# Performance work log

Measured on AMD Instinct MI355X. Metric: run time of the kernel, lower is better.

Reference implementation:

```python
import jax, jax.numpy as jnp
import numpy as np
import math

B, S, D, H, HD, DC, FF, E, K = 4, 2048, 576, 9, 64, 64, 1536, 8, 2
EPS = 1e-6


def _rms(x):
    # RMSNorm with weight=ones (module instantiates a fresh RMSNorm in forward)
    return x / jnp.sqrt(jnp.mean(x * x, axis=-1, keepdims=True) + EPS)


def _expert(h, wa, wb, wc):
    return (jax.nn.gelu(h @ wa, approximate=False) * (h @ wc)) @ wb


def _forward(x, q_w, kv_w, o_w, gate_w, w1, w2, w3, sw1, sw2, sw3):
    # ---------------- MLA ----------------
    xn = _rms(x)
    q = (xn @ q_w).reshape(B, S, H, HD)
    kv = (xn @ kv_w).reshape(B, S, H, 2 * DC)
    k, v = kv[..., :DC], kv[..., DC:]
    # RoPE (complex-pair form) applied to q only, as in the source
    theta = 1.0 / (10000.0 ** (jnp.arange(0, HD, 2, dtype=jnp.float32) / HD))
    freqs = jnp.arange(S, dtype=jnp.float32)[:, None] * theta[None, :]  # [S, HD/2]
    cos = jnp.cos(freqs)[None, :, None, :]
    sin = jnp.sin(freqs)[None, :, None, :]
    qp = q.reshape(B, S, H, HD // 2, 2)
    qe, qo = qp[..., 0], qp[..., 1]
    q = jnp.stack([qe * cos - qo * sin, qe * sin + qo * cos], axis=-1).reshape(B, S, H, HD)
    # NOTE: source matmul attends head-vs-head per token: [B,S,H,HD] x [B,S,DC,H] -> [B,S,H,H]
    attn = jnp.einsum('bshd,bstd->bsht', q, k) / math.sqrt(HD)
    attn = jax.nn.softmax(attn, axis=-1)
    ao = jnp.einsum('bsht,bstd->bshd', attn, v)  # [B,S,H,DC]
    # faithful to torch: transpose(1,2).contiguous().view(B,S,D)
    ao = ao.transpose(0, 2, 1, 3).reshape(B, S, D)
    x = ao @ o_w + x
    # ---------------- MoE ----------------
    xn = _rms(x)
    gw = jax.nn.softmax(xn @ gate_w, axis=-1)  # [B,S,E]
    tw, ti = jax.lax.top_k(gw, K)
    tw = tw / jnp.sum(tw, axis=-1, keepdims=True)
    # combine weights per expert: zero for unselected experts (same math as masked loop)
    comb = jnp.sum(tw[..., None] * jax.nn.one_hot(ti, E, dtype=x.dtype), axis=-2)  # [B,S,E]
    h1 = jax.nn.gelu(jnp.einsum('bsd,edf->ebsf', xn, w1), approximate=False)
    h3 = jnp.einsum('bsd,edf->ebsf', xn, w3)
    eo = jnp.einsum('ebsf,efd->ebsd', h1 * h3, w2)  # [E,B,S,D]
    moe_out = jnp.einsum('ebsd,bse->bsd', eo, comb)
    shared = _expert(xn, sw1, sw2, sw3)
    return moe_out + shared + x


def setup_inputs() -> dict:
    key = jax.random.key(0)
    ks = jax.random.split(key, 11)
    s = 0.02
    return {
        'x': jax.random.normal(ks[0], (B, S, D), dtype=jnp.float32),
        'q_w': jax.random.normal(ks[1], (D, D), dtype=jnp.float32) * s,
        'kv_w': jax.random.normal(ks[2], (D, H * 2 * DC), dtype=jnp.float32) * s,
        'o_w': jax.random.normal(ks[3], (D, D), dtype=jnp.float32) * s,
        'gate_w': jax.random.normal(ks[4], (D, E), dtype=jnp.float32) * s,
        'w1': jax.random.normal(ks[5], (E, D, FF), dtype=jnp.float32) * s,
        'w2': jax.random.normal(ks[6], (E, FF, D), dtype=jnp.float32) * s,
        'w3': jax.random.normal(ks[7], (E, D, FF), dtype=jnp.float32) * s,
        'sw1': jax.random.normal(ks[8], (D, FF), dtype=jnp.float32) * s,
        'sw2': jax.random.normal(ks[9], (FF, D), dtype=jnp.float32) * s,
        'sw3': jax.random.normal(ks[10], (D, FF), dtype=jnp.float32) * s,
    }


def reference(x, q_w, kv_w, o_w, gate_w, w1, w2, w3, sw1, sw2, sw3):
    return _forward(x, q_w, kv_w, o_w, gate_w, w1, w2, w3, sw1, sw2, sw3)
```

## Files before the change

kernel.cpp:

```cpp
#include <hip/hip_runtime.h>
#include <math.h>

#define B_  4
#define S_  2048
#define D_  576
#define H_  9
#define HD_ 64
#define FF_ 1536
#define E_  8
#define TOK (B_*S_)
#define T1ROWS 17408
#define T1ALL  25600

typedef unsigned int   u32x4  __attribute__((ext_vector_type(4)));
typedef unsigned short u16x8  __attribute__((ext_vector_type(8)));
typedef __bf16         bf16x8 __attribute__((ext_vector_type(8)));
typedef _Float16       f16x8  __attribute__((ext_vector_type(8)));
typedef float          f32x4  __attribute__((ext_vector_type(4)));

__device__ __forceinline__ float b2f(unsigned short u) {
    union { unsigned int i; float f; } v; v.i = ((unsigned int)u) << 16; return v.f;
}
__device__ __forceinline__ unsigned short f2b(float f) {
    unsigned int u = __builtin_bit_cast(unsigned int, f);
    unsigned int r = 0x7fffu + ((u >> 16) & 1u);
    return (unsigned short)((u + r) >> 16);
}

__global__ __launch_bounds__(256)
void rmsnorm_k(const float* __restrict__ x, unsigned short* __restrict__ xn) {
    int tok = blockIdx.x, tid = threadIdx.x;
    const float* xr = x + (size_t)tok * D_;
    float v0 = xr[tid];
    float v1 = xr[tid + 256];
    float v2 = (tid < D_ - 512) ? xr[tid + 512] : 0.f;
    float ss = v0*v0 + v1*v1 + v2*v2;
    #pragma unroll
    for (int d = 1; d < 64; d <<= 1) ss += __shfl_xor(ss, d, 64);
    __shared__ float red[4];
    if ((tid & 63) == 0) red[tid >> 6] = ss;
    __syncthreads();
    float tot = red[0] + red[1] + red[2] + red[3];
    float rms = rsqrtf(tot / (float)D_ + 1e-6f);
    unsigned short* orow = xn + (size_t)tok * D_;
    orow[tid]       = f2b(v0 * rms);
    orow[tid + 256] = f2b(v1 * rms);
    if (tid < D_ - 512) orow[tid + 512] = f2b(v2 * rms);
}

__global__ __launch_bounds__(256)
void rms32_k(const float* __restrict__ x, float* __restrict__ xn) {
    int tok = blockIdx.x, tid = threadIdx.x;
    const float* xr = x + (size_t)tok * D_;
    float v0 = xr[tid];
    float v1 = xr[tid + 256];
    float v2 = (tid < D_ - 512) ? xr[tid + 512] : 0.f;
    float ss = v0*v0 + v1*v1 + v2*v2;
    #pragma unroll
    for (int d = 1; d < 64; d <<= 1) ss += __shfl_xor(ss, d, 64);
    __shared__ float red[4];
    if ((tid & 63) == 0) red[tid >> 6] = ss;
    __syncthreads();
    float tot = red[0] + red[1] + red[2] + red[3];
    float rms = rsqrtf(tot / (float)D_ + 1e-6f);
    float* orow = xn + (size_t)tok * D_;
    orow[tid]       = v0 * rms;
    orow[tid + 256] = v1 * rms;
    if (tid < D_ - 512) orow[tid + 512] = v2 * rms;
}

__global__ __launch_bounds__(256)
void convw13_k(const float* __restrict__ w1, const float* __restrict__ w3,
               const float* __restrict__ sw1, const float* __restrict__ sw3,
               unsigned short* __restrict__ wt1, unsigned short* __restrict__ wt3)
{
    const size_t WE = (size_t)D_ * FF_;
    int z = blockIdx.z;
    const float* s; unsigned short* d;
    if (z < 8)       { s = w1 + (size_t)z * WE;       d = wt1 + (size_t)z * WE; }
    else if (z == 8) { s = sw1;                        d = wt1 + 8 * WE; }
    else if (z < 17) { s = w3 + (size_t)(z - 9) * WE;  d = wt3 + (size_t)(z - 9) * WE; }
    else             { s = sw3;                        d = wt3 + 8 * WE; }
    const int K = D_, N = FF_;
    __shared__ unsigned short t[64][72];
    int n0 = blockIdx.x * 64, k0 = blockIdx.y * 64;
    int tx = threadIdx.x & 63, ty = threadIdx.x >> 6;
    #pragma unroll
    for (int i = 0; i < 16; ++i) {
        int k = i * 4 + ty;
        t[k][tx] = f2b(s[(size_t)(k0 + k) * N + n0 + tx]);
    }
    __syncthreads();
    int r = threadIdx.x >> 3, c8 = (threadIdx.x & 7) * 8;
    #pragma unroll
    for (int it = 0; it < 2; ++it, r += 32) {
        u16x8 v;
        #pragma unroll
        for (int j = 0; j < 8; ++j) v[j] = t[c8 + j][r];
        *(u16x8*)&d[(size_t)(n0 + r) * K + k0 + c8] = v;
    }
}

__global__ __launch_bounds__(256)
void convw2_k(const float* __restrict__ w2, const float* __restrict__ sw2,
              unsigned short* __restrict__ wt2)
{
    const size_t WE = (size_t)D_ * FF_;
    int z = blockIdx.z;
    const float* s = (z < 8) ? w2 + (size_t)z * WE : sw2;
    unsigned short* d = wt2 + (size_t)z * WE;
    const int K = FF_, N = D_;
    __shared__ unsigned short t[64][72];
    int n0 = blockIdx.x * 64, k0 = blockIdx.y * 64;
    int tx = threadIdx.x & 63, ty = threadIdx.x >> 6;
    #pragma unroll
    for (int i = 0; i < 16; ++i) {
        int k = i * 4 + ty;
        t[k][tx] = f2b(s[(size_t)(k0 + k) * N + n0 + tx]);
    }
    __syncthreads();
    int r = threadIdx.x >> 3, c8 = (threadIdx.x & 7) * 8;
    #pragma unroll
    for (int it = 0; it < 2; ++it, r += 32) {
        u16x8 v;
        #pragma unroll
        for (int j = 0; j < 8; ++j) v[j] = t[c8 + j][r];
        *(u16x8*)&d[(size_t)(n0 + r) * K + k0 + c8] = v;
    }
}

__global__ __launch_bounds__(256)
void convS_k(const float* __restrict__ src,
             _Float16* __restrict__ dh, _Float16* __restrict__ dl,
             int K, int N)
{
    __shared__ _Float16 th[64][72], tl[64][72];
    int n0 = blockIdx.x * 64, k0 = blockIdx.y * 64;
    int tx = threadIdx.x & 63, ty = threadIdx.x >> 6;
    #pragma unroll
    for (int i = 0; i < 16; ++i) {
        int k = i * 4 + ty;
        float v = src[(size_t)(k0 + k) * N + n0 + tx];
        _Float16 h = (_Float16)v;
        th[k][tx] = h;
        tl[k][tx] = (_Float16)((v - (float)h) * 2048.0f);
    }
    __syncthreads();
    int r = threadIdx.x >> 3, c8 = (threadIdx.x & 7) * 8;
    #pragma unroll
    for (int it = 0; it < 2; ++it, r += 32) {
        f16x8 vh, vl;
        #pragma unroll
        for (int j = 0; j < 8; ++j) { vh[j] = th[c8 + j][r]; vl[j] = tl[c8 + j][r]; }
        *(f16x8*)&dh[(size_t)(n0 + r) * K + k0 + c8] = vh;
        *(f16x8*)&dl[(size_t)(n0 + r) * K + k0 + c8] = vl;
    }
}

template<int BN, int EPI, int WB>
__global__ __launch_bounds__(256)
void gemmS_k(const float* __restrict__ A, const float* __restrict__ Bm,
             const _Float16* __restrict__ Bhp, const _Float16* __restrict__ Blp,
             float* __restrict__ Cout, const float* __restrict__ resid,
             int M, int N, int K, int ldb)
{
    constexpr int BM = 128, BK = 64;
    constexpr int WM = BM / 2, WN = BN / 2, MI = WM / 16, NJ = WN / 16;
    __shared__ alignas(16) _Float16 Ah[BM][BK], Al[BM][BK];
    __shared__ alignas(16) _Float16 Bh[BN][BK], Bl[BN][BK];
    const int tid  = threadIdx.x;
    const int bn0  = blockIdx.x * BN, bm0 = blockIdx.y * BM;
    const int lane = tid & 63, wave = tid >> 6;
    const int l    = lane & 15, quad = lane >> 4;
    const int wm   = wave >> 1, wn = wave & 1;
    const int rsz  = (l & 7) << 3;

    f32x4 accH[MI][NJ], accL[MI][NJ];
    #pragma unroll
    for (int mi = 0; mi < MI; ++mi)
        #pragma unroll
        for (int nj = 0; nj < NJ; ++nj) {
            accH[mi][nj] = (f32x4){0.f, 0.f, 0.f, 0.f};
            accL[mi][nj] = (f32x4){0.f, 0.f, 0.f, 0.f};
        }

    const int nK = K / BK;
    for (int kc = 0; kc < nK; ++kc) {
        __syncthreads();
        #pragma unroll
        for (int i = 0; i < (BM * BK) / 2048; ++i) {
            int u = i * 256 + tid;
            int r = u >> 3, c8 = (u & 7) * 8;
            int cs = c8 ^ ((r & 7) << 3);
            const float* ga = A + (size_t)(bm0 + r) * K + kc * BK + c8;
            f16x8 hh, ll;
            #pragma unroll
            for (int j = 0; j < 8; ++j) {
                float v = ga[j];
                _Float16 h = (_Float16)v;
                hh[j] = h;
                ll[j] = (_Float16)((v - (float)h) * 2048.0f);
            }
            *(f16x8*)&Ah[r][cs] = hh;
            *(f16x8*)&Al[r][cs] = ll;
        }
        if constexpr (WB == 1) {
            #pragma unroll
            for (int i = 0; i < (BN * BK) / 2048; ++i) {
                int u = i * 256 + tid;
                int n = u >> 3, c8 = (u & 7) * 8;
                int cs = c8 ^ ((n & 7) << 3);
                *(f16x8*)&Bh[n][cs] =
                    *(const f16x8*)(Bhp + (size_t)(bn0 + n) * K + kc * BK + c8);
                *(f16x8*)&Bl[n][cs] =
                    *(const f16x8*)(Blp + (size_t)(bn0 + n) * K + kc * BK + c8);
            }
        } else {
            #pragma unroll
            for (int i = 0; i < (BN * BK) / 2048; ++i) {
                int u = i * 256 + tid;
                int n = u % BN, k8 = (u / BN) * 8;
                int cs = k8 ^ ((n & 7) << 3);
                const float* gB = Bm + (size_t)(kc * BK + k8) * ldb + bn0 + n;
                f16x8 hh, ll;
                #pragma unroll
                for (int j = 0; j < 8; ++j) {
                    float v = gB[(size_t)j * ldb];
                    _Float16 h = (_Float16)v;
                    hh[j] = h;
                    ll[j] = (_Float16)((v - (float)h) * 2048.0f);
                }
                *(f16x8*)&Bh[n][cs] = hh;
                *(f16x8*)&Bl[n][cs] = ll;
            }
        }
        __syncthreads();
        #pragma unroll
        for (int ks = 0; ks < BK; ks += 32) {
            f16x8 ah[MI], al[MI], bh[NJ], bl[NJ];
            int col = (ks + quad * 8) ^ rsz;
            #pragma unroll
            for (int mi = 0; mi < MI; ++mi) {
                ah[mi] = *(const f16x8*)&Ah[wm * WM + mi * 16 + l][col];
                al[mi] = *(const f16x8*)&Al[wm * WM + mi * 16 + l][col];
            }
            #pragma unroll
            for (int nj = 0; nj < NJ; ++nj) {
                bh[nj] = *(const f16x8*)&Bh[wn * WN + nj * 16 + l][col];
                bl[nj] = *(const f16x8*)&Bl[wn * WN + nj * 16 + l][col];
            }
            #pragma unroll
            for (int mi = 0; mi < MI; ++mi)
                #pragma unroll
                for (int nj = 0; nj < NJ; ++nj) {
                    accH[mi][nj] = __builtin_amdgcn_mfma_f32_16x16x32_f16(
                        ah[mi], bh[nj], accH[mi][nj], 0, 0, 0);
                    accL[mi][nj] = __builtin_amdgcn_mfma_f32_16x16x32_f16(
                        ah[mi], bl[nj], accL[mi][nj], 0, 0, 0);
                    accL[mi][nj] = __builtin_amdgcn_mfma_f32_16x16x32_f16(
                        al[mi], bh[nj], accL[mi][nj], 0, 0, 0);
                }
        }
    }
    #pragma unroll
    for (int mi = 0; mi < MI; ++mi)
        #pragma unroll
        for (int nj = 0; nj < NJ; ++nj)
            #pragma unroll
            for (int r = 0; r < 4; ++r) {
                int row = bm0 + wm * WM + mi * 16 + quad * 4 + r;
                int col = bn0 + wn * WN + nj * 16 + l;
                float v = accH[mi][nj][r] + accL[mi][nj][r] * (1.0f / 2048.0f);
                size_t idx = (size_t)row * N + col;
                if constexpr (EPI == 0) Cout[idx] = v;
                else                    Cout[idx] = v + resid[idx];
            }
}

__global__ __launch_bounds__(256, 2)
void gemm13_k(const unsigned short* __restrict__ A,
              const unsigned short* __restrict__ B1,
              const unsigned short* __restrict__ B3,
              unsigned short* __restrict__ T1o,
              const int* __restrict__ eidx,
              const int* __restrict__ counts,
              const int* __restrict__ offs,
              int N, long long bstr)
{
    constexpr int BM = 128, BK = 64;
    constexpr int MI = 4, NJ = 4;
    __shared__ alignas(16) unsigned short As[BM][BK];
    __shared__ alignas(16) unsigned short Bs1[BM][BK];
    __shared__ alignas(16) unsigned short Bs3[BM][BK];
    __shared__ int rowbuf[BM];
    const int tid  = threadIdx.x;
    const int bn0  = blockIdx.x * 128, bm0 = blockIdx.y * 128;
    const int lane = tid & 63, wave = tid >> 6;
    const int l    = lane & 15, quad = lane >> 4;
    const int wm   = wave >> 1, wn = wave & 1;
    const int rs   = tid >> 3, c8 = (tid & 7) * 8;
    const int wsz  = (rs & 7) << 3;
    const int rsz  = (l & 7) << 3;

    int e = blockIdx.z;
    int cnt = counts[e];
    if (bm0 >= cnt) return;
    int crow0 = offs[e];
    B1 += (long long)e * bstr;
    B3 += (long long)e * bstr;
    if (tid < BM) {
        int rr = bm0 + tid;
        rowbuf[tid] = (rr < cnt) ? eidx[e * TOK + rr] : 0;
    }
    __syncthreads();

    f32x4 acc1[MI][NJ], acc3[MI][NJ];
    #pragma unroll
    for (int mi = 0; mi < MI; ++mi)
        #pragma unroll
        for (int nj = 0; nj < NJ; ++nj) {
            acc1[mi][nj] = (f32x4){0.f, 0.f, 0.f, 0.f};
            acc3[mi][nj] = (f32x4){0.f, 0.f, 0.f, 0.f};
        }

    const int nK = D_ / BK;
    u32x4 ra[4], rb1[4], rb3[4];
    #pragma unroll
    for (int i = 0; i < 4; ++i) {
        int r = i * 32 + rs;
        int arow = rowbuf[r];
        ra[i]  = *(const u32x4*)(A  + (size_t)arow * D_ + c8);
        rb1[i] = *(const u32x4*)(B1 + (size_t)(bn0 + r) * D_ + c8);
        rb3[i] = *(const u32x4*)(B3 + (size_t)(bn0 + r) * D_ + c8);
    }
    for (int kc = 0; kc < nK; ++kc) {
        __syncthreads();
        #pragma unroll
        for (int i = 0; i < 4; ++i) {
            int r = i * 32 + rs;
            *(u32x4*)&As[r][c8 ^ wsz]  = ra[i];
            *(u32x4*)&Bs1[r][c8 ^ wsz] = rb1[i];
            *(u32x4*)&Bs3[r][c8 ^ wsz] = rb3[i];
        }
        __syncthreads();
        if (kc + 1 < nK) {
            int ko = (kc + 1) * BK;
            #pragma unroll
            for (int i = 0; i < 4; ++i) {
                int r = i * 32 + rs;
                int arow = rowbuf[r];
                ra[i]  = *(const u32x4*)(A  + (size_t)arow * D_ + ko + c8);
                rb1[i] = *(const u32x4*)(B1 + (size_t)(bn0 + r) * D_ + ko + c8);
                rb3[i] = *(const u32x4*)(B3 + (size_t)(bn0 + r) * D_ + ko + c8);
            }
        }
        #pragma unroll
        for (int ks = 0; ks < BK; ks += 32) {
            bf16x8 af[MI], b1f[NJ], b3f[NJ];
            int col = (ks + quad * 8) ^ rsz;
            #pragma unroll
            for (int mi = 0; mi < MI; ++mi)
                af[mi] = __builtin_bit_cast(bf16x8,
                    *(const u32x4*)&As[wm * 64 + mi * 16 + l][col]);
            #pragma unroll
            for (int nj = 0; nj < NJ; ++nj) {
                b1f[nj] = __builtin_bit_cast(bf16x8,
                    *(const u32x4*)&Bs1[wn * 64 + nj * 16 + l][col]);
                b3f[nj] = __builtin_bit_cast(bf16x8,
                    *(const u32x4*)&Bs3[wn * 64 + nj * 16 + l][col]);
            }
            #pragma unroll
            for (int mi = 0; mi < MI; ++mi)
                #pragma unroll
                for (int nj = 0; nj < NJ; ++nj) {
                    acc1[mi][nj] = __builtin_amdgcn_mfma_f32_16x16x32_bf16(
                        af[mi], b1f[nj], acc1[mi][nj], 0, 0, 0);
                    acc3[mi][nj] = __builtin_amdgcn_mfma_f32_16x16x32_bf16(
                        af[mi], b3f[nj], acc3[mi][nj], 0, 0, 0);
                }
        }
    }
    #pragma unroll
    for (int mi = 0; mi < MI; ++mi)
        #pragma unroll
        for (int nj = 0; nj < NJ; ++nj)
            #pragma unroll
            for (int r = 0; r < 4; ++r) {
                int lrow = bm0 + wm * 64 + mi * 16 + quad * 4 + r;
                int col  = bn0 + wn * 64 + nj * 16 + l;
                float hv = b2f(f2b(acc1[mi][nj][r]));
                float g  = 0.5f * hv * (1.0f + erff(hv * 0.70710678118654752f));
                T1o[(size_t)(crow0 + lrow) * N + col] = f2b(g * acc3[mi][nj][r]);
            }
}

__global__ __launch_bounds__(256)
void gemm2_k(const unsigned short* __restrict__ A,
             const unsigned short* __restrict__ Bm,
             float* __restrict__ Cout,
             const float* __restrict__ wgt,
             const int* __restrict__ eidx,
             const int* __restrict__ counts,
             const int* __restrict__ offs,
             int N, int K, int ldb, long long bstr)
{
    constexpr int BM = 64, BN = 192, BK = 64;
    constexpr int MI = 2, NJ = 6;
    constexpr int AIT = (BM * BK) / 2048;
    constexpr int BIT = (BN * BK) / 2048;
    __shared__ alignas(16) unsigned short As[BM][BK];
    __shared__ alignas(16) unsigned short Bs[BN][BK];
    __shared__ int rowbuf[BM];
    const int tid  = threadIdx.x;
    const int bn0  = blockIdx.x * BN, bm0 = blockIdx.y * BM;
    const int lane = tid & 63, wave = tid >> 6;
    const int l    = lane & 15, quad = lane >> 4;
    const int wm   = wave >> 1, wn = wave & 1;
    const int rs   = tid >> 3, c8 = (tid & 7) * 8;
    const int wsz  = (rs & 7) << 3;
    const int rsz  = (l & 7) << 3;

    int e = blockIdx.z;
    int cnt = counts[e];
    if (bm0 >= cnt) return;
    int crow0 = offs[e];
    int ebase = e * TOK;
    const unsigned short* Bt = Bm + (long long)e * bstr;
    if (tid < BM) {
        int rr = bm0 + tid;
        rowbuf[tid] = (rr < cnt) ? eidx[ebase + rr] : 0;
    }

    f32x4 acc[MI][NJ];
    #pragma unroll
    for (int mi = 0; mi < MI; ++mi)
        #pragma unroll
        for (int nj = 0; nj < NJ; ++nj) acc[mi][nj] = (f32x4){0.f, 0.f, 0.f, 0.f};

    const int nK = K / BK;
    u32x4 pa[AIT], pb[BIT];
    #pragma unroll
    for (int i = 0; i < AIT; ++i) {
        int r = i * 32 + rs;
        pa[i] = *(const u32x4*)(A + (size_t)(crow0 + bm0 + r) * K + c8);
    }
    #pragma unroll
    for (int i = 0; i < BIT; ++i) {
        int n = i * 32 + rs;
        pb[i] = *(const u32x4*)(Bt + (size_t)(bn0 + n) * ldb + c8);
    }
    for (int kc = 0; kc < nK; ++kc) {
        __syncthreads();
        #pragma unroll
        for (int i = 0; i < AIT; ++i) {
            int r = i * 32 + rs;
            *(u32x4*)&As[r][c8 ^ wsz] = pa[i];
        }
        #pragma unroll
        for (int i = 0; i < BIT; ++i) {
            int n = i * 32 + rs;
            *(u32x4*)&Bs[n][c8 ^ wsz] = pb[i];
        }
        __syncthreads();
        if (kc + 1 < nK) {
            int ko = (kc + 1) * BK;
            #pragma unroll
            for (int i = 0; i < AIT; ++i) {
                int r = i * 32 + rs;
                pa[i] = *(const u32x4*)(A + (size_t)(crow0 + bm0 + r) * K + ko + c8);
            }
            #pragma unroll
            for (int i = 0; i < BIT; ++i) {
                int n = i * 32 + rs;
                pb[i] = *(const u32x4*)(Bt + (size_t)(bn0 + n) * ldb + ko + c8);
            }
        }
        #pragma unroll
        for (int ks = 0; ks < BK; ks += 32) {
            bf16x8 af[MI], bfr[NJ];
            int col = (ks + quad * 8) ^ rsz;
            #pragma unroll
            for (int mi = 0; mi < MI; ++mi)
                af[mi] = __builtin_bit_cast(bf16x8,
                    *(const u32x4*)&As[wm * 32 + mi * 16 + l][col]);
            #pragma unroll
            for (int nj = 0; nj < NJ; ++nj)
                bfr[nj] = __builtin_bit_cast(bf16x8,
                    *(const u32x4*)&Bs[wn * 96 + nj * 16 + l][col]);
            #pragma unroll
            for (int mi = 0; mi < MI; ++mi)
                #pragma unroll
                for (int nj = 0; nj < NJ; ++nj)
                    acc[mi][nj] = __builtin_amdgcn_mfma_f32_16x16x32_bf16(
                        af[mi], bfr[nj], acc[mi][nj], 0, 0, 0);
        }
    }
    #pragma unroll
    for (int mi = 0; mi < MI; ++mi)
        #pragma unroll
        for (int nj = 0; nj < NJ; ++nj)
            #pragma unroll
            for (int r = 0; r < 4; ++r) {
                int lrow = bm0 + wm * 32 + mi * 16 + quad * 4 + r;
                if (lrow < cnt) {
                    int   tok = rowbuf[lrow - bm0];
                    float sc  = wgt[ebase + lrow];
                    int   col = bn0 + wn * 96 + nj * 16 + l;
                    atomicAdd(&Cout[(size_t)tok * N + col], sc * acc[mi][nj][r]);
                }
            }
}

template<int BN, int EPI, int ROUTED, int WB>
__global__ __launch_bounds__(256)
void gemm_k(const unsigned short* __restrict__ A,
            const void* __restrict__ Bm,
            void* __restrict__ Cout,
            const void* __restrict__ resid,
            const float* __restrict__ wgt,
            const int* __restrict__ eidx,
            const int* __restrict__ counts,
            const int* __restrict__ offs,
            int M, int N, int K, int ldb, long long bstr)
{
    constexpr int BM = 128, BK = 64, LDT = BK + 8;
    constexpr int WM = BM / 2, WN = BN / 2, MI = WM / 16, NJ = WN / 16;
    constexpr int AIT = (BM * BK) / 2048, BIT = (BN * BK) / 2048;
    __shared__ alignas(16) unsigned short As[BM][LDT];
    __shared__ alignas(16) unsigned short Bs[BN][LDT];
    __shared__ int rowbuf[BM];
    const int tid  = threadIdx.x;
    const int bn0  = blockIdx.x * BN, bm0 = blockIdx.y * BM;
    const int lane = tid & 63, wave = tid >> 6;
    const int l    = lane & 15, quad = lane >> 4;
    const int wm   = wave >> 1, wn = wave & 1;

    int cnt = M, crow0 = 0, ebase = 0;
    long long boff = 0;
    if constexpr (ROUTED) {
        int e = blockIdx.z;
        cnt = counts[e];
        if (bm0 >= cnt) return;
        crow0 = offs[e];
        ebase = e * TOK;
        boff  = (long long)e * bstr;
        if (tid < BM) {
            int rr = bm0 + tid;
            rowbuf[tid] = (rr < cnt) ? eidx[ebase + rr] : 0;
        }
        __syncthreads();
    }

    f32x4 acc[MI][NJ];
    #pragma unroll
    for (int mi = 0; mi < MI; ++mi)
        #pragma unroll
        for (int nj = 0; nj < NJ; ++nj) acc[mi][nj] = (f32x4){0.f, 0.f, 0.f, 0.f};

    const int nK = K / BK;
    for (int kc = 0; kc < nK; ++kc) {
        __syncthreads();
        #pragma unroll
        for (int i = 0; i < AIT; ++i) {
            int u = i * 256 + tid;
            int r = u >> 3, c8 = (u & 7) * 8;
            int arow;
            if constexpr (ROUTED && EPI != 5) arow = rowbuf[r];
            else if constexpr (ROUTED)        arow = crow0 + bm0 + r;
            else                              arow = bm0 + r;
            *(u32x4*)&As[r][c8] =
                *(const u32x4*)(A + (size_t)arow * K + kc * BK + c8);
        }
        const float* Bf = (const float*)Bm + boff;
        #pragma unroll
        for (int i = 0; i < BIT; ++i) {
            int u = i * 256 + tid;
            int n = u % BN, k8 = (u / BN) * 8;
            const float* gB = Bf + (size_t)(kc * BK + k8) * ldb + bn0 + n;
            u16x8 tmp;
            #pragma unroll
            for (int j = 0; j < 8; ++j) tmp[j] = f2b(gB[(size_t)j * ldb]);
            *(u16x8*)&Bs[n][k8] = tmp;
        }
        __syncthreads();
        #pragma unroll
        for (int ks = 0; ks < BK; ks += 32) {
            bf16x8 af[MI], bfr[NJ];
            #pragma unroll
            for (int mi = 0; mi < MI; ++mi)
                af[mi] = __builtin_bit_cast(bf16x8,
                    *(const u32x4*)&As[wm * WM + mi * 16 + l][ks + quad * 8]);
            #pragma unroll
            for (int nj = 0; nj < NJ; ++nj)
                bfr[nj] = __builtin_bit_cast(bf16x8,
                    *(const u32x4*)&Bs[wn * WN + nj * 16 + l][ks + quad * 8]);
            #pragma unroll
            for (int mi = 0; mi < MI; ++mi)
                #pragma unroll
                for (int nj = 0; nj < NJ; ++nj)
                    acc[mi][nj] = __builtin_amdgcn_mfma_f32_16x16x32_bf16(
                        af[mi], bfr[nj], acc[mi][nj], 0, 0, 0);
        }
    }
    #pragma unroll
    for (int mi = 0; mi < MI; ++mi)
        #pragma unroll
        for (int nj = 0; nj < NJ; ++nj)
            #pragma unroll
            for (int r = 0; r < 4; ++r) {
                int lrow = bm0 + wm * WM + mi * 16 + quad * 4 + r;
                int col  = bn0 + wn * WN + nj * 16 + l;
                float v = acc[mi][nj][r];
                if constexpr (EPI == 0) {
                    ((unsigned short*)Cout)[(size_t)(crow0 + lrow) * N + col] = f2b(v);
                } else if constexpr (EPI == 3) {
                    size_t ix = (size_t)(crow0 + lrow) * N + col;
                    float hv = b2f(((const unsigned short*)resid)[ix]);
                    float g = 0.5f * hv * (1.0f + erff(hv * 0.70710678118654752f));
                    ((unsigned short*)Cout)[ix] = f2b(g * v);
                } else if constexpr (EPI == 4) {
                    ((float*)Cout)[(size_t)lrow * N + col] += v;
                } else {
                    if (lrow < cnt) {
                        int   tok = rowbuf[lrow - bm0];
                        float sc  = wgt[ebase + lrow];
                        atomicAdd(&((float*)Cout)[(size_t)tok * N + col], sc * v);
                    }
                }
            }
}

__global__ __launch_bounds__(256)
void attn32_k(const float* __restrict__ q,
              const float* __restrict__ kv,
              float* __restrict__ ao,
              int pos0)
{
    int pl   = blockIdx.x * 4 + (threadIdx.x >> 6);
    int lane = threadIdx.x & 63;
    int pos  = pos0 + pl;
    int b = pos >> 11, s = pos & 2047;

    const float* qp  = q  + (size_t)pl * 576;
    const float* kvp = kv + (size_t)pl * 1152;

    int i = lane >> 1;
    float theta = powf(10000.f, -(float)i * (1.0f / 32.0f));
    float sn, cs;
    sincosf((float)s * theta, &sn, &cs);

    float qr[H_], kr[H_], vr[H_];
    #pragma unroll
    for (int h = 0; h < H_; ++h) {
        float qv = qp[h * 64 + lane];
        float qo = __shfl_xor(qv, 1, 64);
        qr[h] = (lane & 1) ? (qo * sn + qv * cs) : (qv * cs - qo * sn);
        kr[h] = kvp[h * 128 + lane];
        vr[h] = kvp[h * 128 + 64 + lane];
    }

    #pragma unroll
    for (int h = 0; h < H_; ++h) {
        float sc[H_];
        #pragma unroll
        for (int t = 0; t < H_; ++t) {
            float p = qr[h] * kr[t];
            #pragma unroll
            for (int d = 1; d < 64; d <<= 1) p += __shfl_xor(p, d, 64);
            sc[t] = p * 0.125f;
        }
        float mx = sc[0];
        #pragma unroll
        for (int t = 1; t < H_; ++t) mx = fmaxf(mx, sc[t]);
        float ssum = 0.f;
        #pragma unroll
        for (int t = 0; t < H_; ++t) { sc[t] = __expf(sc[t] - mx); ssum += sc[t]; }
        float inv = 1.0f / ssum;
        float ov = 0.f;
        #pragma unroll
        for (int t = 0; t < H_; ++t) ov += sc[t] * vr[t];
        ao[((size_t)(b * H_ + h) * S_ + s) * 64 + lane] = ov * inv;
    }
}

__global__ __launch_bounds__(256)
void gate1_k(const float* __restrict__ x2,
             const float* __restrict__ gw,
             float* __restrict__ tw,
             int*   __restrict__ tsel)
{
    int tok  = blockIdx.x * 4 + (threadIdx.x >> 6);
    int lane = threadIdx.x & 63;
    float acc[8];
    #pragma unroll
    for (int e = 0; e < 8; ++e) acc[e] = 0.f;
    float ss = 0.f;
    for (int d = lane; d < D_; d += 64) {
        float xv = x2[(size_t)tok * D_ + d];
        ss += xv * xv;
        const float* wr = gw + (size_t)d * 8;
        #pragma unroll
        for (int e = 0; e < 8; ++e) acc[e] += xv * wr[e];
    }
    #pragma unroll
    for (int d = 1; d < 64; d <<= 1) ss += __shfl_xor(ss, d, 64);
    #pragma unroll
    for (int e = 0; e < 8; ++e)
        #pragma unroll
        for (int d = 1; d < 64; d <<= 1) acc[e] += __shfl_xor(acc[e], d, 64);
    if (lane == 0) {
        float rms = rsqrtf(ss / (float)D_ + 1e-6f);
        #pragma unroll
        for (int e = 0; e < 8; ++e) acc[e] *= rms;
        float mx = acc[0];
        #pragma unroll
        for (int e = 1; e < 8; ++e) mx = fmaxf(mx, acc[e]);
        float g[8], ssum = 0.f;
        #pragma unroll
        for (int e = 0; e < 8; ++e) { g[e] = __expf(acc[e] - mx); ssum += g[e]; }
        #pragma unroll
        for (int e = 0; e < 8; ++e) g[e] /= ssum;
        int i1 = 0;
        #pragma unroll
        for (int e = 1; e < 8; ++e) if (g[e] > g[i1]) i1 = e;
        int i2 = -1;
        #pragma unroll
        for (int e = 0; e < 8; ++e)
            if (e != i1 && (i2 < 0 || g[e] > g[i2])) i2 = e;
        float s2 = g[i1] + g[i2];
        tw[(size_t)tok * 2 + 0] = g[i1] / s2;
        tw[(size_t)tok * 2 + 1] = g[i2] / s2;
        tsel[tok] = i1 | (i2 << 8);
    }
}

__global__ __launch_bounds__(256)
void gate2_k(const int*   __restrict__ tsel,
             const float* __restrict__ tw,
             float* __restrict__ wgt,
             int*   __restrict__ eidx,
             int*   __restrict__ counts)
{
    int e    = blockIdx.x;
    int tid  = threadIdx.x;
    int lane = tid & 63, wv = tid >> 6;
    __shared__ int wtot[4];
    int base = 0;
    for (int t0 = 0; t0 < TOK; t0 += 256) {
        int tok = t0 + tid;
        int hit = 0; float w = 0.f;
        if (e == E_) { hit = 1; w = 1.0f; }
        else {
            int s = tsel[tok];
            if ((s & 255) == e)      { hit = 1; w = tw[(size_t)tok * 2 + 0]; }
            else if ((s >> 8) == e)  { hit = 1; w = tw[(size_t)tok * 2 + 1]; }
        }
        unsigned long long m = __ballot(hit);
        int pre = __popcll(m & ((1ull << lane) - 1ull));
        if (lane == 0) wtot[wv] = __popcll(m);
        __syncthreads();
        int off = base;
        for (int q = 0; q < wv; ++q) off += wtot[q];
        if (hit) {
            int p = off + pre;
            eidx[e * TOK + p] = tok;
            wgt [e * TOK + p] = w;
        }
        base += wtot[0] + wtot[1] + wtot[2] + wtot[3];
        __syncthreads();
    }
    if (tid == 0) counts[e] = base;
}

__global__ void offs_k(const int* __restrict__ counts, int* __restrict__ offs) {
    if (threadIdx.x == 0) {
        int run = 0;
        for (int e = 0; e < 9; ++e) {
            offs[e] = run;
            run += ((counts[e] + 127) >> 7) << 7;
        }
    }
}

extern "C" void kernel_launch(void* const* d_in, const int* in_sizes, int n_in,
                              void* d_out, int out_size, void* d_ws, size_t ws_size,
                              hipStream_t stream)
{
    const float* x      = (const float*)d_in[0];
    const float* q_w    = (const float*)d_in[1];
    const float* kv_w   = (const float*)d_in[2];
    const float* o_w    = (const float*)d_in[3];
    const float* gate_w = (const float*)d_in[4];
    const float* w1     = (const float*)d_in[5];
    const float* w2     = (const float*)d_in[6];
    const float* w3     = (const float*)d_in[7];
    const float* sw1    = (const float*)d_in[8];
    const float* sw2    = (const float*)d_in[9];
    const float* sw3    = (const float*)d_in[10];
    float* out = (float*)d_out;

    const size_t XN = (size_t)TOK * D_ * 2;
    char* ws = (char*)d_ws;
    unsigned short* xn16 = (unsigned short*)ws;
    float*          ao32 = (float*)(ws + XN);

    const size_t QE = (size_t)D_ * D_, KVE = (size_t)1152 * D_;
    const size_t SW = (2 * QE + KVE) * 2 * 2;
    _Float16* qwh  = (_Float16*)(ws + 3 * XN);
    _Float16* qwl  = qwh  + QE;
    _Float16* kvwh = qwl  + QE;
    _Float16* kvwl = kvwh + KVE;
    _Float16* owh  = kvwl + KVE;
    _Float16* owl  = owh  + QE;

    bool convA = true;
    int TC = -1;
    for (int pass = 0; pass < 2; ++pass) {
        size_t base = 3 * XN + (convA ? SW : 0);
        if      (base + 8*XN    <= ws_size) { TC = 1; break; }
        else if (base + 8*XN/2  <= ws_size) { TC = 2; break; }
        else if (base + 8*XN/4  <= ws_size) { TC = 4; break; }
        else if (base + 8*XN/8  <= ws_size) { TC = 8; break; }
        else if (base + 8*XN/16 <= ws_size) { TC = 16; break; }
        else if (base + 8*XN/32 <= ws_size) { TC = 32; break; }
        else if (base + 8*XN/64 <= ws_size) { TC = 64; break; }
        convA = false;
    }
    if (TC < 0) { convA = false; TC = 64; }
    const int CT = TOK / TC;
    float* xn32c = (float*)(ws + 3*XN + (convA ? SW : 0));
    float* qc    = xn32c + (size_t)CT * D_;
    float* kvc   = qc    + (size_t)CT * D_;

    int*   counts = (int*)(ws + XN);
    int*   offs   = counts + 16;
    float* wgt    = (float*)(ws + XN + 256);
    int*   eidx   = (int*)  (ws + XN + 256 + (size_t)9 * TOK * 4);
    float* tw     = (float*)(ws + XN + 256 + (size_t)9 * TOK * 8);
    int*   tsel   = (int*)  (ws + XN + 256 + (size_t)9 * TOK * 8 + (size_t)TOK * 8);
    const size_t fixedG = XN + 256 + (size_t)9 * TOK * 8 + (size_t)TOK * 12;

    const size_t WELEM = (size_t)D_ * FF_;
    const size_t WSZ   = 27 * WELEM * 2;

    bool conv; int FC;
    if      (fixedG + WSZ + (size_t)T1ALL * FF_     * 2 <= ws_size) { conv = true;  FC = 1; }
    else if (fixedG + WSZ + (size_t)T1ALL * (FF_/2) * 2 <= ws_size) { conv = true;  FC = 2; }
    else if (fixedG + WSZ + (size_t)T1ALL * (FF_/4) * 2 <= ws_size) { conv = true;  FC = 4; }
    else if (fixedG + (size_t)T1ROWS * FF_     * 2 <= ws_size)      { conv = false; FC = 1; }
    else if (fixedG + (size_t)T1ROWS * (FF_/2) * 2 <= ws_size)      { conv = false; FC = 2; }
    else                                                            { conv = false; FC = 4; }
    const int FFc = FF_ / FC;

    unsigned short* wt1 = (unsigned short*)(ws + fixedG);
    unsigned short* wt3 = wt1 + 9 * WELEM;
    unsigned short* wt2 = wt3 + 9 * WELEM;
    unsigned short* t1  = (unsigned short*)(ws + fixedG + (conv ? WSZ : 0));

    if (convA) {
        convS_k<<<dim3(D_/64,  D_/64), 256, 0, stream>>>(q_w,  qwh,  qwl,  D_, D_);
        convS_k<<<dim3(1152/64, D_/64), 256, 0, stream>>>(kv_w, kvwh, kvwl, D_, 1152);
        convS_k<<<dim3(D_/64,  D_/64), 256, 0, stream>>>(o_w,  owh,  owl,  D_, D_);
    }
    for (int t = 0; t < TC; ++t) {
        const float* xc = x + (size_t)t * CT * D_;
        rms32_k<<<CT, 256, 0, stream>>>(xc, xn32c);
        if (convA) {
            gemmS_k<64, 0, 1><<<dim3(D_ / 64, CT / 128), 256, 0, stream>>>(
                xn32c, nullptr, qwh, qwl, qc, nullptr, CT, D_, D_, D_);
            gemmS_k<64, 0, 1><<<dim3(1152 / 64, CT / 128), 256, 0, stream>>>(
                xn32c, nullptr, kvwh, kvwl, kvc, nullptr, CT, 1152, D_, D_);
        } else {
            gemmS_k<64, 0, 0><<<dim3(D_ / 64, CT / 128), 256, 0, stream>>>(
                xn32c, q_w, nullptr, nullptr, qc, nullptr, CT, D_, D_, D_);
            gemmS_k<64, 0, 0><<<dim3(1152 / 64, CT / 128), 256, 0, stream>>>(
                xn32c, kv_w, nullptr, nullptr, kvc, nullptr, CT, 1152, D_, 1152);
        }
        attn32_k<<<CT / 4, 256, 0, stream>>>(qc, kvc, ao32, t * CT);
    }
    if (convA)
        gemmS_k<64, 1, 1><<<dim3(D_ / 64, TOK / 128), 256, 0, stream>>>(
            ao32, nullptr, owh, owl, out, x, TOK, D_, D_, D_);
    else
        gemmS_k<64, 1, 0><<<dim3(D_ / 64, TOK / 128), 256, 0, stream>>>(
            ao32, o_w, nullptr, nullptr, out, x, TOK, D_, D_, D_);
    rmsnorm_k<<<TOK, 256, 0, stream>>>(out, xn16);
    gate1_k<<<TOK / 4, 256, 0, stream>>>(out, gate_w, tw, tsel);
    gate2_k<<<E_ + 1, 256, 0, stream>>>(tsel, tw, wgt, eidx, counts);
    offs_k<<<1, 64, 0, stream>>>(counts, offs);
    if (conv) {
        convw13_k<<<dim3(FF_/64, D_/64, 18), 256, 0, stream>>>(
            w1, w3, sw1, sw3, wt1, wt3);
        convw2_k<<<dim3(D_/64, FF_/64, 9), 256, 0, stream>>>(w2, sw2, wt2);
    }
    for (int c = 0; c < FC; ++c) {
        if (conv) {
            gemm13_k<<<dim3(FFc / 128, TOK / 128, 9), 256, 0, stream>>>(
                xn16, wt1 + (size_t)c * FFc * D_, wt3 + (size_t)c * FFc * D_,
                t1, eidx, counts, offs, FFc, (long long)WELEM);
            gemm2_k<<<dim3(D_ / 192, TOK / 64, 9), 256, 0, stream>>>(
                t1, wt2 + (size_t)c * FFc, out, wgt, eidx, counts, offs,
                D_, FFc, FF_, (long long)WELEM);
        } else {
            const float* w1c = w1 + (size_t)c * FFc;
            const float* w3c = w3 + (size_t)c * FFc;
            const float* w2c = w2 + (size_t)c * FFc * D_;
            gemm_k<128, 0, 1, 0><<<dim3(FFc / 128, TOK / 128, E_), 256, 0, stream>>>(
                xn16, w1c, t1, nullptr, wgt, eidx, counts, offs,
                TOK, FFc, D_, FF_, (long long)D_ * FF_);
            gemm_k<128, 3, 1, 0><<<dim3(FFc / 128, TOK / 128, E_), 256, 0, stream>>>(
                xn16, w3c, t1, t1, wgt, eidx, counts, offs,
                TOK, FFc, D_, FF_, (long long)D_ * FF_);
            gemm_k<64, 5, 1, 0><<<dim3(D_ / 64, TOK / 128, E_), 256, 0, stream>>>(
                t1, w2c, out, nullptr, wgt, eidx, counts, offs,
                TOK, D_, FFc, D_, (long long)FF_ * D_);
            gemm_k<128, 0, 0, 0><<<dim3(FFc / 128, TOK / 128), 256, 0, stream>>>(
                xn16, sw1 + (size_t)c * FFc, t1, nullptr, nullptr, nullptr, nullptr, nullptr,
                TOK, FFc, D_, FF_, 0);
            gemm_k<128, 3, 0, 0><<<dim3(FFc / 128, TOK / 128), 256, 0, stream>>>(
                xn16, sw3 + (size_t)c * FFc, t1, t1, nullptr, nullptr, nullptr, nullptr,
                TOK, FFc, D_, FF_, 0);
            gemm_k<64, 4, 0, 0><<<dim3(D_ / 64, TOK / 128), 256, 0, stream>>>(
                t1, sw2 + (size_t)c * FFc * D_, out, nullptr, nullptr, nullptr, nullptr, nullptr,
                TOK, D_, FFc, D_, 0);
        }
    }
}
```

Before: 634.2 us.

## Pre-split normalized activations into fp16 hi/lo and swizzle GEMM block order

A new RMSNorm kernel writes the normalized activations directly as fp16 high and scaled-low halves. The Q and KV GEMMs then load these halves straight into shared memory instead of each re-reading fp32 and recomputing the split, which removes redundant conversion work and halves the A-operand bytes per GEMM. A 2D block-index swizzle that groups workgroups in strides of eight is also added to all GEMMs to change tile visit order for cache locality. The risk is that the swizzle could hurt locality for some grid shapes.

```diff
diff --git a/kernel.cpp b/kernel.cpp
--- a/kernel.cpp
+++ b/kernel.cpp
@@ -27,6 +27,17 @@
     return (unsigned short)((u + r) >> 16);
 }
 
+__device__ __forceinline__ void swz2d(int& bx, int& by) {
+    int nx = gridDim.x, ny = gridDim.y;
+    int nwg = nx * ny;
+    if ((nwg & 7) == 0) {
+        int orig = by * nx + bx;
+        int logical = (orig & 7) * (nwg >> 3) + (orig >> 3);
+        bx = logical % nx;
+        by = logical / nx;
+    }
+}
+
 __global__ __launch_bounds__(256)
 void rmsnorm_k(const float* __restrict__ x, unsigned short* __restrict__ xn) {
     int tok = blockIdx.x, tid = threadIdx.x;
@@ -67,6 +78,38 @@
     orow[tid]       = v0 * rms;
     orow[tid + 256] = v1 * rms;
     if (tid < D_ - 512) orow[tid + 512] = v2 * rms;
+}
+
+__global__ __launch_bounds__(256)
+void rmssplit_k(const float* __restrict__ x,
+                _Float16* __restrict__ xh, _Float16* __restrict__ xl) {
+    int tok = blockIdx.x, tid = threadIdx.x;
+    const float* xr = x + (size_t)tok * D_;
+    float v0 = xr[tid];
+    float v1 = xr[tid + 256];
+    float v2 = (tid < D_ - 512) ? xr[tid + 512] : 0.f;
+    float ss = v0*v0 + v1*v1 + v2*v2;
+    #pragma unroll
+    for (int d = 1; d < 64; d <<= 1) ss += __shfl_xor(ss, d, 64);
+    __shared__ float red[4];
+    if ((tid & 63) == 0) red[tid >> 6] = ss;
+    __syncthreads();
+    float tot = red[0] + red[1] + red[2] + red[3];
+    float rms = rsqrtf(tot / (float)D_ + 1e-6f);
+    _Float16* hr = xh + (size_t)tok * D_;
+    _Float16* lr = xl + (size_t)tok * D_;
+    {
+        float v = v0 * rms; _Float16 h = (_Float16)v;
+        hr[tid] = h; lr[tid] = (_Float16)((v - (float)h) * 2048.0f);
+    }
+    {
+        float v = v1 * rms; _Float16 h = (_Float16)v;
+        hr[tid + 256] = h; lr[tid + 256] = (_Float16)((v - (float)h) * 2048.0f);
+    }
+    if (tid < D_ - 512) {
+        float v = v2 * rms; _Float16 h = (_Float16)v;
+        hr[tid + 512] = h; lr[tid + 512] = (_Float16)((v - (float)h) * 2048.0f);
+    }
 }
 
 __global__ __launch_bounds__(256)
@@ -157,9 +200,11 @@
     }
 }
 
-template<int BN, int EPI, int WB>
-__global__ __launch_bounds__(256)
-void gemmS_k(const float* __restrict__ A, const float* __restrict__ Bm,
+template<int BN, int EPI, int WB, int AB>
+__global__ __launch_bounds__(256)
+void gemmS_k(const float* __restrict__ A,
+             const _Float16* __restrict__ Ahp, const _Float16* __restrict__ Alp,
+             const float* __restrict__ Bm,
              const _Float16* __restrict__ Bhp, const _Float16* __restrict__ Blp,
              float* __restrict__ Cout, const float* __restrict__ resid,
              int M, int N, int K, int ldb)
@@ -169,7 +214,9 @@
     __shared__ alignas(16) _Float16 Ah[BM][BK], Al[BM][BK];
     __shared__ alignas(16) _Float16 Bh[BN][BK], Bl[BN][BK];
     const int tid  = threadIdx.x;
-    const int bn0  = blockIdx.x * BN, bm0 = blockIdx.y * BM;
+    int bxi = blockIdx.x, byi = blockIdx.y;
+    swz2d(bxi, byi);
+    const int bn0  = bxi * BN, bm0 = byi * BM;
     const int lane = tid & 63, wave = tid >> 6;
     const int l    = lane & 15, quad = lane >> 4;
     const int wm   = wave >> 1, wn = wave & 1;
@@ -187,22 +234,35 @@
     const int nK = K / BK;
     for (int kc = 0; kc < nK; ++kc) {
         __syncthreads();
-        #pragma unroll
-        for (int i = 0; i < (BM * BK) / 2048; ++i) {
-            int u = i * 256 + tid;
-            int r = u >> 3, c8 = (u & 7) * 8;
-            int cs = c8 ^ ((r & 7) << 3);
-            const float* ga = A + (size_t)(bm0 + r) * K + kc * BK + c8;
-            f16x8 hh, ll;
-            #pragma unroll
-            for (int j = 0; j < 8; ++j) {
-                float v = ga[j];
-                _Float16 h = (_Float16)v;
-                hh[j] = h;
-                ll[j] = (_Float16)((v - (float)h) * 2048.0f);
-            }
-            *(f16x8*)&Ah[r][cs] = hh;
-            *(f16x8*)&Al[r][cs] = ll;
+        if constexpr (AB == 1) {
+            #pragma unroll
+            for (int i = 0; i < (BM * BK) / 2048; ++i) {
+                int u = i * 256 + tid;
+                int r = u >> 3, c8 = (u & 7) * 8;
+                int cs = c8 ^ ((r & 7) << 3);
+                *(f16x8*)&Ah[r][cs] =
+                    *(const f16x8*)(Ahp + (size_t)(bm0 + r) * K + kc * BK + c8);
+                *(f16x8*)&Al[r][cs] =
+                    *(const f16x8*)(Alp + (size_t)(bm0 + r) * K + kc * BK + c8);
+            }
+        } else {
+            #pragma unroll
+            for (int i = 0; i < (BM * BK) / 2048; ++i) {
+                int u = i * 256 + tid;
+                int r = u >> 3, c8 = (u & 7) * 8;
+                int cs = c8 ^ ((r & 7) << 3);
+                const float* ga = A + (size_t)(bm0 + r) * K + kc * BK + c8;
+                f16x8 hh, ll;
+                #pragma unroll
+                for (int j = 0; j < 8; ++j) {
+                    float v = ga[j];
+                    _Float16 h = (_Float16)v;
+                    hh[j] = h;
+                    ll[j] = (_Float16)((v - (float)h) * 2048.0f);
+                }
+                *(f16x8*)&Ah[r][cs] = hh;
+                *(f16x8*)&Al[r][cs] = ll;
+            }
         }
         if constexpr (WB == 1) {
             #pragma unroll
@@ -294,7 +354,9 @@
     __shared__ alignas(16) unsigned short Bs3[BM][BK];
     __shared__ int rowbuf[BM];
     const int tid  = threadIdx.x;
-    const int bn0  = blockIdx.x * 128, bm0 = blockIdx.y * 128;
+    int bxi = blockIdx.x, byi = blockIdx.y;
+    swz2d(bxi, byi);
+    const int bn0  = bxi * 128, bm0 = byi * 128;
     const int lane = tid & 63, wave = tid >> 6;
     const int l    = lane & 15, quad = lane >> 4;
     const int wm   = wave >> 1, wn = wave & 1;
@@ -412,7 +474,9 @@
     __shared__ alignas(16) unsigned short Bs[BN][BK];
     __shared__ int rowbuf[BM];
     const int tid  = threadIdx.x;
-    const int bn0  = blockIdx.x * BN, bm0 = blockIdx.y * BM;
+    int bxi = blockIdx.x, byi = blockIdx.y;
+    swz2d(bxi, byi);
+    const int bn0  = bxi * BN, bm0 = byi * BM;
     const int lane = tid & 63, wave = tid >> 6;
     const int l    = lane & 15, quad = lane >> 4;
     const int wm   = wave >> 1, wn = wave & 1;
@@ -828,9 +892,12 @@
     }
     if (TC < 0) { convA = false; TC = 64; }
     const int CT = TOK / TC;
-    float* xn32c = (float*)(ws + 3*XN + (convA ? SW : 0));
-    float* qc    = xn32c + (size_t)CT * D_;
-    float* kvc   = qc    + (size_t)CT * D_;
+    char* chunk0 = ws + 3*XN + (convA ? SW : 0);
+    _Float16* xnh  = (_Float16*)chunk0;
+    _Float16* xnl  = xnh + (size_t)CT * D_;
+    float*    xn32c = (float*)chunk0;
+    float*    qc   = (float*)(chunk0 + (size_t)CT * D_ * 4);
+    float*    kvc  = qc + (size_t)CT * D_;
 
     int*   counts = (int*)(ws + XN);
     int*   offs   = counts + 16;
@@ -864,26 +931,27 @@
     }
     for (int t = 0; t < TC; ++t) {
         const float* xc = x + (size_t)t * CT * D_;
-        rms32_k<<<CT, 256, 0, stream>>>(xc, xn32c);
         if (convA) {
-            gemmS_k<64, 0, 1><<<dim3(D_ / 64, CT / 128), 256, 0, stream>>>(
-                xn32c, nullptr, qwh, qwl, qc, nullptr, CT, D_, D_, D_);
-            gemmS_k<64, 0, 1><<<dim3(1152 / 64, CT / 128), 256, 0, stream>>>(
-                xn32c, nullptr, kvwh, kvwl, kvc, nullptr, CT, 1152, D_, D_);
+            rmssplit_k<<<CT, 256, 0, stream>>>(xc, xnh, xnl);
+            gemmS_k<64, 0, 1, 1><<<dim3(D_ / 64, CT / 128), 256, 0, stream>>>(
+                nullptr, xnh, xnl, nullptr, qwh, qwl, qc, nullptr, CT, D_, D_, D_);
+            gemmS_k<64, 0, 1, 1><<<dim3(1152 / 64, CT / 128), 256, 0, stream>>>(
+                nullptr, xnh, xnl, nullptr, kvwh, kvwl, kvc, nullptr, CT, 1152, D_, D_);
         } else {
-            gemmS_k<64, 0, 0><<<dim3(D_ / 64, CT / 128), 256, 0, stream>>>(
-                xn32c, q_w, nullptr, nullptr, qc, nullptr, CT, D_, D_, D_);
-            gemmS_k<64, 0, 0><<<dim3(1152 / 64, CT / 128), 256, 0, stream>>>(
-                xn32c, kv_w, nullptr, nullptr, kvc, nullptr, CT, 1152, D_, 1152);
+            rms32_k<<<CT, 256, 0, stream>>>(xc, xn32c);
+            gemmS_k<64, 0, 0, 0><<<dim3(D_ / 64, CT / 128), 256, 0, stream>>>(
+                xn32c, nullptr, nullptr, q_w, nullptr, nullptr, qc, nullptr, CT, D_, D_, D_);
+            gemmS_k<64, 0, 0, 0><<<dim3(1152 / 64, CT / 128), 256, 0, stream>>>(
+                xn32c, nullptr, nullptr, kv_w, nullptr, nullptr, kvc, nullptr, CT, 1152, D_, 1152);
         }
         attn32_k<<<CT / 4, 256, 0, stream>>>(qc, kvc, ao32, t * CT);
     }
     if (convA)
-        gemmS_k<64, 1, 1><<<dim3(D_ / 64, TOK / 128), 256, 0, stream>>>(
-            ao32, nullptr, owh, owl, out, x, TOK, D_, D_, D_);
+        gemmS_k<64, 1, 1, 0><<<dim3(D_ / 64, TOK / 128), 256, 0, stream>>>(
+            ao32, nullptr, nullptr, nullptr, owh, owl, out, x, TOK, D_, D_, D_);
     else
-        gemmS_k<64, 1, 0><<<dim3(D_ / 64, TOK / 128), 256, 0, stream>>>(
-            ao32, o_w, nullptr, nullptr, out, x, TOK, D_, D_, D_);
+        gemmS_k<64, 1, 0, 0><<<dim3(D_ / 64, TOK / 128), 256, 0, stream>>>(
+            ao32, nullptr, nullptr, o_w, nullptr, nullptr, out, x, TOK, D_, D_, D_);
     rmsnorm_k<<<TOK, 256, 0, stream>>>(out, xn16);
     gate1_k<<<TOK / 4, 256, 0, stream>>>(out, gate_w, tw, tsel);
     gate2_k<<<E_ + 1, 256, 0, stream>>>(tsel, tw, wgt, eidx, counts);
```

After: 877.5 us. 38.4% more time.
